# Performance work log

Measured on AMD Instinct MI355X. Metric: run time of the kernel, lower is better.

## Reference

```python
import jax, jax.numpy as jnp
import numpy as np

H = 128   # hidden_size
B = 8
TQ = 512  # num queries
TK = 512  # num keys


def setup_inputs() -> dict:
    key = jax.random.key(0)
    ks = jax.random.split(key, 8)
    s = 1.0 / np.sqrt(H)  # torch Linear default init bound
    return {
        "queries": jax.random.normal(ks[0], (B, TQ, H), dtype=jnp.float32),
        "keys": jax.random.normal(ks[1], (B, TK, H), dtype=jnp.float32),
        "Wa_w": jax.random.uniform(ks[2], (H, H), jnp.float32, -s, s),
        "Wa_b": jax.random.uniform(ks[3], (H,), jnp.float32, -s, s),
        "Ua_w": jax.random.uniform(ks[4], (H, H), jnp.float32, -s, s),
        "Ua_b": jax.random.uniform(ks[5], (H,), jnp.float32, -s, s),
        "Va_w": jax.random.uniform(ks[6], (H,), jnp.float32, -s, s),
        "Va_b": jax.random.uniform(ks[7], (), jnp.float32, -s, s),
    }


def reference(queries, keys, Wa_w, Wa_b, Ua_w, Ua_b, Va_w, Va_b):
    # Linear projections (torch Linear: y = x @ W.T + b)
    q = queries @ Wa_w.T + Wa_b                  # (B, Tq, H)
    k = keys @ Ua_w.T + Ua_b                     # (B, Tk, H)
    # Additive (Bahdanau) scores with broadcast intermediate (B, Tq, Tk, H)
    e = jnp.tanh(q[:, :, None, :] + k[:, None, :, :])
    scores = jnp.einsum('bqkh,h->bqk', e, Va_w) + Va_b  # (B, Tq, Tk)
    weights = jax.nn.softmax(scores, axis=-1)            # softmax over keys
    contexts = jnp.einsum('bqk,bkh->bqh', weights, keys) # (B, Tq, H)
    return contexts, weights
```

## Files before the change

### kernel.cpp

```cpp
#include <hip/hip_runtime.h>
#include <hip/hip_bf16.h>
#include <stdint.h>

#define HD 128
#define NB 8
#define TQN 512
#define TKN 512
#define QT 8
#define KTILE 64
#define KSTR 132
#define QSTR 132
#define KBSTR 136
#define FQT 8

typedef __attribute__((ext_vector_type(8))) short short8;
typedef __attribute__((ext_vector_type(4))) float f32x4;
typedef __attribute__((ext_vector_type(2))) float f32x2;

#if __has_builtin(__builtin_elementwise_fma)
#define FMA2(a,b,c) __builtin_elementwise_fma((a),(b),(c))
#else
#define FMA2(a,b,c) ((a)*(b)+(c))
#endif

static __device__ __forceinline__ float lo16(uint32_t w){
  union { uint32_t i; float f; } v; v.i = w << 16; return v.f;
}
static __device__ __forceinline__ float hi16(uint32_t w){
  union { uint32_t i; float f; } v; v.i = w & 0xffff0000u; return v.f;
}
static __device__ __forceinline__ float bf2f(unsigned short u){
  union { uint32_t i; float f; } v; v.i = ((uint32_t)u) << 16; return v.f;
}
static __device__ __forceinline__ uint32_t f2bf(float f){
  union { float f; uint32_t i; } v; v.f = f;
  uint32_t u = v.i;
  u += 0x7fffu + ((u >> 16) & 1u);
  return u >> 16;
}
static __device__ __forceinline__ float tanh_acc(float x){
  float e = __builtin_amdgcn_exp2f(x * 2.8853900817779268f);
  return fmaf(-2.0f, __builtin_amdgcn_rcpf(e + 1.0f), 1.0f);
}
template<int CTRL>
static __device__ __forceinline__ float dpp_add(float x){
  union { float f; int i; } u; u.f = x;
  int y = __builtin_amdgcn_update_dpp(0, u.i, CTRL, 0xf, 0xf, true);
  union { int i; float f; } w; w.i = y;
  return x + w.f;
}
static __device__ __forceinline__ float ld1(const void* p, size_t idx, bool f32){
  return f32 ? ((const float*)p)[idx] : bf2f(((const unsigned short*)p)[idx]);
}
static __device__ __forceinline__ short8 ld8bf(const void* p, size_t idx, bool f32){
  short8 r;
  if (f32){
    const float* s = (const float*)p + idx;
    #pragma unroll
    for (int i = 0; i < 8; i++) r[i] = (short)f2bf(s[i]);
  } else {
    r = *(const short8*)((const unsigned short*)p + idx);
  }
  return r;
}

__global__ __launch_bounds__(256) void proj_kernel(
    const void* __restrict__ queries, const void* __restrict__ keys,
    const void* __restrict__ Wa_w,   const void* __restrict__ Wa_b,
    const void* __restrict__ Ua_w,   const void* __restrict__ Ua_b,
    float* __restrict__ tq_g, float* __restrict__ tk_g)
{
  __shared__ unsigned int flg_s[8];
  const int tid = threadIdx.x;
  if (tid < 8) flg_s[tid] = 0;
  __syncthreads();
  {
    const void* ptrs[6] = {queries, keys, Wa_w, Wa_b, Ua_w, Ua_b};
    const int grp = tid >> 5;
    const int l   = tid & 31;
    if (grp < 6){
      const unsigned short* p = (const unsigned short*)ptrs[grp];
      unsigned short a = p[2*l], c = p[64 + 2*l];
      if (((a >> 7) & 0xFF) > 0x90 || ((c >> 7) & 0xFF) > 0x90)
        atomicOr(&flg_s[grp], 1u);
    }
  }
  __syncthreads();
  const int lane = tid & 63, wv = tid >> 6, ln = lane & 15, quad = lane >> 4;
  const int b7  = blockIdx.x & 7;
  const int idx = blockIdx.x >> 3;
  const int row0 = (idx < 32) ? (b7*TQN + idx*16)
                              : (NB*TQN + b7*TKN + (idx-32)*16);

  const void* x; const void* W; const void* bias; float* dst; int r;
  bool fx, fw, fb;
  if (row0 < NB*TQN){
    x = queries; W = Wa_w; bias = Wa_b; dst = tq_g; r = row0;
    fx = flg_s[0] != 0; fw = flg_s[2] != 0; fb = flg_s[3] != 0;
  } else {
    x = keys; W = Ua_w; bias = Ua_b; dst = tk_g; r = row0 - NB*TQN;
    fx = flg_s[1] != 0; fw = flg_s[4] != 0; fb = flg_s[5] != 0;
  }

  short8 a[4];
  #pragma unroll
  for (int ks = 0; ks < 4; ks++)
    a[ks] = ld8bf(x, (size_t)(r + ln)*HD + ks*32 + quad*8, fx);

  #pragma unroll
  for (int nt = 0; nt < 2; nt++){
    const int h0 = (2*wv + nt)*16;
    f32x4 c = {0.f,0.f,0.f,0.f};
    #pragma unroll
    for (int ks = 0; ks < 4; ks++)
      c = __builtin_amdgcn_mfma_f32_16x16x32_bf16(
            a[ks], ld8bf(W, (size_t)(h0 + ln)*HD + ks*32 + quad*8, fw), c, 0,0,0);
    const float wb = ld1(bias, h0 + ln, fb);
    #pragma unroll
    for (int r4 = 0; r4 < 4; r4++){
      const float e = __builtin_amdgcn_exp2f((c[r4] + wb) * 2.8853900817779268f);
      dst[(size_t)(r + quad*4 + r4)*HD + h0 + ln] =
          fminf(fmaxf(e, 0x1p-13f), 0x1p13f);
    }
  }
}

__global__ __launch_bounds__(1024, 8) void attn_kernel(
    const void* __restrict__ queries, const void* __restrict__ keys,
    const void* __restrict__ Va_w,
    const float* __restrict__ tq_g, const float* __restrict__ tk_g,
    void* __restrict__ out)
{
  __shared__ __align__(16) float tk_s[KTILE*KSTR];
  __shared__ float wgt_s[QT*TKN];
  __shared__ unsigned int flg_s[4];

  const int tid = threadIdx.x;
  const int b     = blockIdx.x & 7;
  const int qbase = (blockIdx.x >> 3) * QT;

  float4 st[2];
  {
    const float4* src = (const float4*)(tk_g + (size_t)(b*TKN)*HD);
    #pragma unroll
    for (int j = 0; j < 2; j++) st[j] = src[tid + 1024*j];
  }

  if (tid < 4) flg_s[tid] = 0;
  __syncthreads();
  {
    const void* ptrs[3] = {queries, keys, Va_w};
    const int grp = tid >> 5;
    const int l   = tid & 31;
    if (grp < 3){
      const unsigned short* p = (const unsigned short*)ptrs[grp];
      unsigned short a = p[2*l], c = p[64 + 2*l];
      if (((a >> 7) & 0xFF) > 0x90 || ((c >> 7) & 0xFF) > 0x90)
        atomicOr(&flg_s[grp], 1u);
    }
  }
  __syncthreads();
  const bool fQ  = flg_s[0] != 0;
  const bool fK  = flg_s[1] != 0;
  const bool fVw = flg_s[2] != 0;

  const int lane = tid & 63;
  const int wv   = tid >> 6;
  const int qr   = wv & 7;
  const int hh   = wv >> 3;
  const int ln   = lane & 15;
  const int quad = lane >> 4;
  const int s8   = lane >> 3;
  const int o8   = lane & 7;

  f32x2 eq2[4], a2[4];
  {
    const float* qsrc = tq_g + (size_t)(b*TQN + qbase + qr)*HD + o8*16 + hh*8;
    #pragma unroll
    for (int c = 0; c < 2; c++){
      const float4 t = *(const float4*)(qsrc + c*4);
      eq2[2*c].x = t.x; eq2[2*c].y = t.y;
      eq2[2*c+1].x = t.z; eq2[2*c+1].y = t.w;
      a2[2*c].x   = -2.0f * ld1(Va_w, o8*16 + hh*8 + c*4 + 0, fVw);
      a2[2*c].y   = -2.0f * ld1(Va_w, o8*16 + hh*8 + c*4 + 1, fVw);
      a2[2*c+1].x = -2.0f * ld1(Va_w, o8*16 + hh*8 + c*4 + 2, fVw);
      a2[2*c+1].y = -2.0f * ld1(Va_w, o8*16 + hh*8 + c*4 + 3, fVw);
    }
  }
  f32x2 one2; one2.x = 1.f; one2.y = 1.f;

  float sc8[8];
  for (int kt = 0; kt < 8; kt++){
    #pragma unroll
    for (int j = 0; j < 2; j++){
      const int f = tid + 1024*j;
      *(float4*)(tk_s + (f >> 5)*KSTR + (f & 31)*4) = st[j];
    }
    __syncthreads();
    if (kt < 7){
      const float4* src = (const float4*)(tk_g + (size_t)(b*TKN + (kt+1)*KTILE)*HD);
      #pragma unroll
      for (int j = 0; j < 2; j++) st[j] = src[tid + 1024*j];
    }

    float acc[8];
    #pragma unroll
    for (int i = 0; i < 8; i++){
      const float* tk = tk_s + (i*8 + s8)*KSTR + o8*16 + hh*8;
      float acci = 0.f;
      #pragma unroll
      for (int c = 0; c < 2; c++){
        const float4 kv = *(const float4*)(tk + c*4);
        f32x2 kv0; kv0.x = kv.x; kv0.y = kv.y;
        f32x2 kv1; kv1.x = kv.z; kv1.y = kv.w;
        f32x2 x01 = FMA2(eq2[2*c],   kv0, one2);
        f32x2 x23 = FMA2(eq2[2*c+1], kv1, one2);
        f32x2 xs01; xs01.x = x01.y; xs01.y = x01.x;
        f32x2 xs23; xs23.x = x23.y; xs23.y = x23.x;
        f32x2 s01 = a2[2*c]   * xs01;
        f32x2 s23 = a2[2*c+1] * xs23;
        const float p01 = x01.x * x01.y;
        const float p23 = x23.x * x23.y;
        const float n01 = s01.x + s01.y;
        const float n23 = s23.x + s23.y;
        const float P   = p01 * p23;
        const float N   = fmaf(n01, p23, n23 * p01);
        acci = fmaf(N, __builtin_amdgcn_rcpf(P), acci);
      }
      acc[i] = acci;
    }
    #pragma unroll
    for (int i = 0; i < 8; i++){
      float a = acc[i];
      a = dpp_add<0xB1>(a);
      a = dpp_add<0x4E>(a);
      a = dpp_add<0x141>(a);
      acc[i] = a;
    }
    float sc = acc[0];
    #pragma unroll
    for (int i = 1; i < 8; i++) sc = (o8 == i) ? acc[i] : sc;
    sc8[kt] = sc;
    __syncthreads();
  }

  if (hh == 1){
    #pragma unroll
    for (int kt = 0; kt < 8; kt++)
      tk_s[qr*TKN + kt*64 + o8*8 + s8] = sc8[kt];
  }
  __syncthreads();
  if (hh == 0){
    float vals[8];
    float m = -1e30f;
    #pragma unroll
    for (int j = 0; j < 8; j++){
      vals[j] = sc8[j] + tk_s[qr*TKN + j*64 + o8*8 + s8];
      m = fmaxf(m, vals[j]);
    }
    #pragma unroll
    for (int o = 32; o > 0; o >>= 1) m = fmaxf(m, __shfl_xor(m, o));
    float sum = 0.f;
    #pragma unroll
    for (int j = 0; j < 8; j++){
      vals[j] = __builtin_amdgcn_exp2f((vals[j]-m)*1.4426950408889634f);
      sum += vals[j];
    }
    #pragma unroll
    for (int o = 32; o > 0; o >>= 1) sum += __shfl_xor(sum, o);
    const float inv = __builtin_amdgcn_rcpf(sum);
    const int psrc = ((((lane & 7) << 3) | (lane >> 3)) << 2);
    const size_t wbase = (size_t)NB*TQN*HD + (size_t)(b*TQN + qbase + qr)*TKN;
    float* wrow = wgt_s + qr*TKN;
    #pragma unroll
    for (int j = 0; j < 8; j++){
      union { float f; int i; } u; u.f = vals[j]*inv;
      union { int i; float f; } t; t.i = __builtin_amdgcn_ds_bpermute(psrc, u.i);
      wrow[j*64 + lane] = t.f;
      if (fQ) ((float*)out)[wbase + j*64 + lane] = t.f;
      else    ((unsigned short*)out)[wbase + j*64 + lane] = (unsigned short)f2bf(t.f);
    }
  }
  __syncthreads();

  {
    const int p2 = wv & 3;
    const int g2 = wv >> 2;
    const int h0 = ln * 8;
    f32x2 a0v[4], a1v[4];
    #pragma unroll
    for (int t = 0; t < 4; t++){
      a0v[t].x = 0.f; a0v[t].y = 0.f;
      a1v[t].x = 0.f; a1v[t].y = 0.f;
    }
    const float* w0rb = wgt_s + (2*p2)*TKN;
    if (!fK){
      const unsigned short* kb = (const unsigned short*)keys
          + (size_t)(b*TKN)*HD + h0;
      #pragma unroll
      for (int t = 0; t < 2; t++){
        const int kt = g2*2 + t;
        const float* w0r = w0rb + kt*KTILE;
        const float* w1r = w0r + TKN;
        #pragma unroll
        for (int i = 0; i < 16; i++){
          const int k = i*4 + quad;
          const uint4 v = *(const uint4*)(kb + (size_t)(kt*KTILE + k)*HD);
          const float w0 = w0r[k];
          const float w1 = w1r[k];
          f32x2 c0; c0.x = lo16(v.x); c0.y = hi16(v.x);
          f32x2 c1; c1.x = lo16(v.y); c1.y = hi16(v.y);
          f32x2 c2; c2.x = lo16(v.z); c2.y = hi16(v.z);
          f32x2 c3; c3.x = lo16(v.w); c3.y = hi16(v.w);
          f32x2 w0v; w0v.x = w0; w0v.y = w0;
          f32x2 w1v; w1v.x = w1; w1v.y = w1;
          a0v[0] = FMA2(w0v, c0, a0v[0]); a0v[1] = FMA2(w0v, c1, a0v[1]);
          a0v[2] = FMA2(w0v, c2, a0v[2]); a0v[3] = FMA2(w0v, c3, a0v[3]);
          a1v[0] = FMA2(w1v, c0, a1v[0]); a1v[1] = FMA2(w1v, c1, a1v[1]);
          a1v[2] = FMA2(w1v, c2, a1v[2]); a1v[3] = FMA2(w1v, c3, a1v[3]);
        }
      }
    } else {
      const float* kb = (const float*)keys + (size_t)(b*TKN)*HD + h0;
      #pragma unroll
      for (int t = 0; t < 2; t++){
        const int kt = g2*2 + t;
        const float* w0r = w0rb + kt*KTILE;
        const float* w1r = w0r + TKN;
        #pragma unroll
        for (int i = 0; i < 16; i++){
          const int k = i*4 + quad;
          const float* kr = kb + (size_t)(kt*KTILE + k)*HD;
          const float4 k0 = *(const float4*)(kr);
          const float4 k1 = *(const float4*)(kr + 4);
          const float w0 = w0r[k];
          const float w1 = w1r[k];
          f32x2 c0; c0.x = k0.x; c0.y = k0.y;
          f32x2 c1; c1.x = k0.z; c1.y = k0.w;
          f32x2 c2; c2.x = k1.x; c2.y = k1.y;
          f32x2 c3; c3.x = k1.z; c3.y = k1.w;
          f32x2 w0v; w0v.x = w0; w0v.y = w0;
          f32x2 w1v; w1v.x = w1; w1v.y = w1;
          a0v[0] = FMA2(w0v, c0, a0v[0]); a0v[1] = FMA2(w0v, c1, a0v[1]);
          a0v[2] = FMA2(w0v, c2, a0v[2]); a0v[3] = FMA2(w0v, c3, a0v[3]);
          a1v[0] = FMA2(w1v, c0, a1v[0]); a1v[1] = FMA2(w1v, c1, a1v[1]);
          a1v[2] = FMA2(w1v, c2, a1v[2]); a1v[3] = FMA2(w1v, c3, a1v[3]);
        }
      }
    }
    float a0[8], a1[8];
    #pragma unroll
    for (int t = 0; t < 4; t++){
      a0[2*t] = a0v[t].x; a0[2*t+1] = a0v[t].y;
      a1[2*t] = a1v[t].x; a1[2*t+1] = a1v[t].y;
    }
    #pragma unroll
    for (int t = 0; t < 8; t++){
      a0[t] += __shfl_xor(a0[t], 16); a0[t] += __shfl_xor(a0[t], 32);
      a1[t] += __shfl_xor(a1[t], 16); a1[t] += __shfl_xor(a1[t], 32);
    }
    float* part = tk_s;
    if (g2 > 0 && quad == 0){
      const int base = ((g2-1)*8 + 2*p2)*HD + h0;
      *(float4*)(part + base       ) = (float4){a0[0],a0[1],a0[2],a0[3]};
      *(float4*)(part + base + 4   ) = (float4){a0[4],a0[5],a0[6],a0[7]};
      *(float4*)(part + base + HD  ) = (float4){a1[0],a1[1],a1[2],a1[3]};
      *(float4*)(part + base + HD+4) = (float4){a1[4],a1[5],a1[6],a1[7]};
    }
    __syncthreads();
    if (g2 == 0 && quad == 0){
      #pragma unroll
      for (int gg = 0; gg < 3; gg++){
        const int base = (gg*8 + 2*p2)*HD + h0;
        const float4 q00 = *(const float4*)(part + base);
        const float4 q01 = *(const float4*)(part + base + 4);
        const float4 q10 = *(const float4*)(part + base + HD);
        const float4 q11 = *(const float4*)(part + base + HD + 4);
        a0[0]+=q00.x; a0[1]+=q00.y; a0[2]+=q00.z; a0[3]+=q00.w;
        a0[4]+=q01.x; a0[5]+=q01.y; a0[6]+=q01.z; a0[7]+=q01.w;
        a1[0]+=q10.x; a1[1]+=q10.y; a1[2]+=q10.z; a1[3]+=q10.w;
        a1[4]+=q11.x; a1[5]+=q11.y; a1[6]+=q11.z; a1[7]+=q11.w;
      }
      const size_t crow0 = (size_t)(b*TQN + qbase + 2*p2    )*HD + h0;
      const size_t crow1 = (size_t)(b*TQN + qbase + 2*p2 + 1)*HD + h0;
      if (fQ){
        float* oc = (float*)out;
        *(float4*)(oc + crow0)     = (float4){a0[0],a0[1],a0[2],a0[3]};
        *(float4*)(oc + crow0 + 4) = (float4){a0[4],a0[5],a0[6],a0[7]};
        *(float4*)(oc + crow1)     = (float4){a1[0],a1[1],a1[2],a1[3]};
        *(float4*)(oc + crow1 + 4) = (float4){a1[4],a1[5],a1[6],a1[7]};
      } else {
        uint4 o0, o1;
        o0.x = f2bf(a0[0]) | (f2bf(a0[1]) << 16);
        o0.y = f2bf(a0[2]) | (f2bf(a0[3]) << 16);
        o0.z = f2bf(a0[4]) | (f2bf(a0[5]) << 16);
        o0.w = f2bf(a0[6]) | (f2bf(a0[7]) << 16);
        o1.x = f2bf(a1[0]) | (f2bf(a1[1]) << 16);
        o1.y = f2bf(a1[2]) | (f2bf(a1[3]) << 16);
        o1.z = f2bf(a1[4]) | (f2bf(a1[5]) << 16);
        o1.w = f2bf(a1[6]) | (f2bf(a1[7]) << 16);
        *(uint4*)((unsigned short*)out + crow0) = o0;
        *(uint4*)((unsigned short*)out + crow1) = o1;
      }
    }
  }
}

__global__ __launch_bounds__(512, 4) void fused_kernel(
    const void* __restrict__ queries, const void* __restrict__ keys,
    const void* __restrict__ Wa_w,   const void* __restrict__ Wa_b,
    const void* __restrict__ Ua_w,   const void* __restrict__ Ua_b,
    const void* __restrict__ Va_w,
    void* __restrict__ out)
{
  __shared__ float qp_s[FQT*QSTR];
  __shared__ float va_s[HD];
  __shared__ __align__(16) unsigned short keys_s[KTILE*KBSTR];
  __shared__ __align__(16) float kp_s[KTILE*QSTR];
  __shared__ float sc_s[FQT*TKN];
  __shared__ unsigned int flg_s[8];

  const int tid = threadIdx.x;
  if (tid < 8) flg_s[tid] = 0;
  __syncthreads();
  {
    const void* ptrs[7] = {queries, keys, Wa_w, Wa_b, Ua_w, Ua_b, Va_w};
    const int grp = tid >> 5;
    const int l   = tid & 31;
    if (grp < 7){
      const unsigned short* p = (const unsigned short*)ptrs[grp];
      unsigned short a = p[2*l], c = p[64 + 2*l];
      if (((a >> 7) & 0xFF) > 0x90 || ((c >> 7) & 0xFF) > 0x90)
        atomicOr(&flg_s[grp], 1u);
    }
  }
  __syncthreads();
  const bool fQ  = flg_s[0] != 0;
  const bool fK  = flg_s[1] != 0;
  const bool fWw = flg_s[2] != 0;
  const bool fWb = flg_s[3] != 0;
  const bool fUw = flg_s[4] != 0;
  const bool fUb = flg_s[5] != 0;
  const bool fVw = flg_s[6] != 0;

  const int lane = tid & 63;
  const int wv   = tid >> 6;
  const int ln   = lane & 15;
  const int quad = lane >> 4;
  const int b     = blockIdx.x >> 6;
  const int qbase = (blockIdx.x & 63) * FQT;

  if (tid < HD) va_s[tid] = ld1(Va_w, tid, fVw);
  {
    const int h0 = wv * 16;
    const size_t qrow = (size_t)(b*TQN + qbase + (ln & 7))*HD;
    f32x4 c = {0.f,0.f,0.f,0.f};
    #pragma unroll
    for (int ks = 0; ks < 4; ks++){
      short8 a = ld8bf(queries, qrow + ks*32 + quad*8, fQ);
      short8 w = ld8bf(Wa_w, (size_t)(h0 + ln)*HD + ks*32 + quad*8, fWw);
      c = __builtin_amdgcn_mfma_f32_16x16x32_bf16(a, w, c, 0,0,0);
    }
    const float wb = ld1(Wa_b, h0 + ln, fWb);
    #pragma unroll
    for (int r = 0; r < 4; r++){
      const int row = quad*4 + r;
      if (row < FQT) qp_s[row*QSTR + h0 + ln] = tanh_acc(c[r] + wb);
    }
  }
  short8 ub[4];
  float ubias;
  {
    const int h0 = wv * 16;
    #pragma unroll
    for (int ks = 0; ks < 4; ks++)
      ub[ks] = ld8bf(Ua_w, (size_t)(h0 + ln)*HD + ks*32 + quad*8, fUw);
    ubias = ld1(Ua_b, h0 + ln, fUb);
  }
  {
    if (fK){
      const float4* src = (const float4*)((const float*)keys + (size_t)(b*TKN)*HD);
      #pragma unroll
      for (int j = 0; j < 4; j++){
        const int f = tid + 512*j;
        float4 v = src[f];
        const int k = f >> 5, h = (f & 31)*4;
        uint2 p;
        p.x = f2bf(v.x) | (f2bf(v.y) << 16);
        p.y = f2bf(v.z) | (f2bf(v.w) << 16);
        *(uint2*)(keys_s + k*KBSTR + h) = p;
      }
    } else {
      const uint4* src = (const uint4*)((const unsigned short*)keys + (size_t)(b*TKN)*HD);
      #pragma unroll
      for (int j = 0; j < 2; j++){
        const int f = tid + 512*j;
        uint4 v = src[f];
        const int k = f >> 4, h = (f & 15)*8;
        *(uint4*)(keys_s + k*KBSTR + h) = v;
      }
    }
  }
  __syncthreads();

  const int s8 = lane >> 3;
  const int o8 = lane & 7;
  float tqr[16], var[16], vat[16];
  {
    const float* qsrc = qp_s + wv*QSTR + o8*16;
    const float* vsrc = va_s + o8*16;
    #pragma unroll
    for (int c = 0; c < 4; c++){
      float4 t = *(const float4*)(qsrc + c*4);
      float4 v = *(const float4*)(vsrc + c*4);
      tqr[c*4+0]=t.x; tqr[c*4+1]=t.y; tqr[c*4+2]=t.z; tqr[c*4+3]=t.w;
      var[c*4+0]=v.x; var[c*4+1]=v.y; var[c*4+2]=v.z; var[c*4+3]=v.w;
      vat[c*4+0]=v.x*t.x; vat[c*4+1]=v.y*t.y; vat[c*4+2]=v.z*t.z; vat[c*4+3]=v.w*t.w;
    }
  }
  for (int kt = 0; kt < 8; kt++){
    f32x4 kc[4];
    #pragma unroll
    for (int mt = 0; mt < 4; mt++) kc[mt] = (f32x4){0.f,0.f,0.f,0.f};
    #pragma unroll
    for (int ks = 0; ks < 4; ks++){
      short8 af[4];
      #pragma unroll
      for (int mt = 0; mt < 4; mt++)
        af[mt] = *(const short8*)(keys_s + (mt*16 + ln)*KBSTR + ks*32 + quad*8);
      #pragma unroll
      for (int mt = 0; mt < 4; mt++)
        kc[mt] = __builtin_amdgcn_mfma_f32_16x16x32_bf16(af[mt], ub[ks], kc[mt], 0,0,0);
    }
    __syncthreads();
    #pragma unroll
    for (int mt = 0; mt < 4; mt++)
      #pragma unroll
      for (int r = 0; r < 4; r++)
        kp_s[(mt*16 + quad*4 + r)*QSTR + wv*16 + ln] = tanh_acc(kc[mt][r] + ubias);
    if (kt < 7){
      if (fK){
        const float4* src = (const float4*)((const float*)keys + (size_t)(b*TKN + (kt+1)*KTILE)*HD);
        #pragma unroll
        for (int j = 0; j < 4; j++){
          const int f = tid + 512*j;
          float4 v = src[f];
          const int k = f >> 5, h = (f & 31)*4;
          uint2 p;
          p.x = f2bf(v.x) | (f2bf(v.y) << 16);
          p.y = f2bf(v.z) | (f2bf(v.w) << 16);
          *(uint2*)(keys_s + k*KBSTR + h) = p;
        }
      } else {
        const uint4* src = (const uint4*)((const unsigned short*)keys + (size_t)(b*TKN + (kt+1)*KTILE)*HD);
        #pragma unroll
        for (int j = 0; j < 2; j++){
          const int f = tid + 512*j;
          uint4 v = src[f];
          const int k = f >> 4, h = (f & 15)*8;
          *(uint4*)(keys_s + k*KBSTR + h) = v;
        }
      }
    }
    __syncthreads();
    float acc[8];
    #pragma unroll
    for (int i = 0; i < 8; i++) acc[i] = 0.f;
    #pragma unroll
    for (int i = 0; i < 8; i++){
      const float* tk = kp_s + (i*8 + s8)*QSTR + o8*16;
      #pragma unroll
      for (int c = 0; c < 4; c++){
        const float4 kv = *(const float4*)(tk + c*4);
        acc[i] = fmaf(fmaf(var[c*4+0], kv.x, vat[c*4+0]),
                      __builtin_amdgcn_rcpf(fmaf(tqr[c*4+0], kv.x, 1.f)), acc[i]);
        acc[i] = fmaf(fmaf(var[c*4+1], kv.y, vat[c*4+1]),
                      __builtin_amdgcn_rcpf(fmaf(tqr[c*4+1], kv.y, 1.f)), acc[i]);
        acc[i] = fmaf(fmaf(var[c*4+2], kv.z, vat[c*4+2]),
                      __builtin_amdgcn_rcpf(fmaf(tqr[c*4+2], kv.z, 1.f)), acc[i]);
        acc[i] = fmaf(fmaf(var[c*4+3], kv.w, vat[c*4+3]),
                      __builtin_amdgcn_rcpf(fmaf(tqr[c*4+3], kv.w, 1.f)), acc[i]);
      }
    }
    #pragma unroll
    for (int i = 0; i < 8; i++){
      float a = acc[i];
      a = dpp_add<0xB1>(a);
      a = dpp_add<0x4E>(a);
      a = dpp_add<0x141>(a);
      acc[i] = a;
    }
    float sc = acc[0];
    #pragma unroll
    for (int i = 1; i < 8; i++) sc = (o8 == i) ? acc[i] : sc;
    sc_s[wv*TKN + kt*KTILE + o8*8 + s8] = sc;
  }
  __syncthreads();
  {
    float vals[8];
    float m = -1e30f;
    #pragma unroll
    for (int j = 0; j < 8; j++){
      vals[j] = sc_s[wv*TKN + lane + 64*j];
      m = fmaxf(m, vals[j]);
    }
    #pragma unroll
    for (int o = 32; o > 0; o >>= 1) m = fmaxf(m, __shfl_xor(m, o));
    float sum = 0.f;
    #pragma unroll
    for (int j = 0; j < 8; j++){
      vals[j] = __builtin_amdgcn_exp2f((vals[j]-m)*1.4426950408889634f);
      sum += vals[j];
    }
    #pragma unroll
    for (int o = 32; o > 0; o >>= 1) sum += __shfl_xor(sum, o);
    const float inv = __builtin_amdgcn_rcpf(sum);
    const size_t wbase = (size_t)NB*TQN*HD + (size_t)(b*TQN + qbase + wv)*TKN;
    #pragma unroll
    for (int j = 0; j < 8; j++){
      const float w = vals[j]*inv;
      sc_s[wv*TKN + lane + 64*j] = w;
      if (fQ) ((float*)out)[wbase + lane + 64*j] = w;
      else    ((unsigned short*)out)[wbase + lane + 64*j] = (unsigned short)f2bf(w);
    }
  }
  __syncthreads();
  {
    const int p2 = wv & 3;
    const int g2 = wv >> 2;
    const int h0 = ln * 8;
    float a0[8], a1[8];
    #pragma unroll
    for (int t = 0; t < 8; t++){ a0[t] = 0.f; a1[t] = 0.f; }
    for (int kt = 0; kt < 8; kt++){
      if (fK){
        const float4* src = (const float4*)((const float*)keys + (size_t)(b*TKN + kt*KTILE)*HD);
        #pragma unroll
        for (int j = 0; j < 4; j++){
          const int f = tid + 512*j;
          const int k = f >> 5, h = (f & 31)*4;
          *(float4*)(kp_s + k*QSTR + h) = src[f];
        }
      } else {
        const uint4* src = (const uint4*)((const unsigned short*)keys + (size_t)(b*TKN + kt*KTILE)*HD);
        #pragma unroll
        for (int j = 0; j < 2; j++){
          const int f = tid + 512*j;
          const int k = f >> 4, h = (f & 15)*8;
          uint4 v = src[f];
          float4 d0, d1;
          d0.x = lo16(v.x); d0.y = hi16(v.x); d0.z = lo16(v.y); d0.w = hi16(v.y);
          d1.x = lo16(v.z); d1.y = hi16(v.z); d1.z = lo16(v.w); d1.w = hi16(v.w);
          *(float4*)(kp_s + k*QSTR + h)     = d0;
          *(float4*)(kp_s + k*QSTR + h + 4) = d1;
        }
      }
      __syncthreads();
      const float* w0r = sc_s + (2*p2)*TKN + kt*KTILE + g2*32;
      const float* w1r = w0r + TKN;
      #pragma unroll
      for (int i = 0; i < 8; i++){
        const int k = i*4 + quad;
        const float w0 = w0r[k];
        const float w1 = w1r[k];
        const float* kr = kp_s + (g2*32 + k)*QSTR + h0;
        const float4 k0 = *(const float4*)(kr);
        const float4 k1 = *(const float4*)(kr + 4);
        a0[0]=fmaf(w0,k0.x,a0[0]); a0[1]=fmaf(w0,k0.y,a0[1]);
        a0[2]=fmaf(w0,k0.z,a0[2]); a0[3]=fmaf(w0,k0.w,a0[3]);
        a0[4]=fmaf(w0,k1.x,a0[4]); a0[5]=fmaf(w0,k1.y,a0[5]);
        a0[6]=fmaf(w0,k1.z,a0[6]); a0[7]=fmaf(w0,k1.w,a0[7]);
        a1[0]=fmaf(w1,k0.x,a1[0]); a1[1]=fmaf(w1,k0.y,a1[1]);
        a1[2]=fmaf(w1,k0.z,a1[2]); a1[3]=fmaf(w1,k0.w,a1[3]);
        a1[4]=fmaf(w1,k1.x,a1[4]); a1[5]=fmaf(w1,k1.y,a1[5]);
        a1[6]=fmaf(w1,k1.z,a1[6]); a1[7]=fmaf(w1,k1.w,a1[7]);
      }
      __syncthreads();
    }
    #pragma unroll
    for (int t = 0; t < 8; t++){
      a0[t] += __shfl_xor(a0[t], 16); a0[t] += __shfl_xor(a0[t], 32);
      a1[t] += __shfl_xor(a1[t], 16); a1[t] += __shfl_xor(a1[t], 32);
    }
    float* part = qp_s;
    if (g2 == 1 && quad == 0){
      *(float4*)(part + (2*p2  )*HD + h0    ) = (float4){a0[0],a0[1],a0[2],a0[3]};
      *(float4*)(part + (2*p2  )*HD + h0 + 4) = (float4){a0[4],a0[5],a0[6],a0[7]};
      *(float4*)(part + (2*p2+1)*HD + h0    ) = (float4){a1[0],a1[1],a1[2],a1[3]};
      *(float4*)(part + (2*p2+1)*HD + h0 + 4) = (float4){a1[4],a1[5],a1[6],a1[7]};
    }
    __syncthreads();
    if (g2 == 0 && quad == 0){
      const float4 p00 = *(const float4*)(part + (2*p2  )*HD + h0    );
      const float4 p01 = *(const float4*)(part + (2*p2  )*HD + h0 + 4);
      const float4 p10 = *(const float4*)(part + (2*p2+1)*HD + h0    );
      const float4 p11 = *(const float4*)(part + (2*p2+1)*HD + h0 + 4);
      const size_t crow0 = (size_t)(b*TQN + qbase + 2*p2    )*HD + h0;
      const size_t crow1 = (size_t)(b*TQN + qbase + 2*p2 + 1)*HD + h0;
      if (fQ){
        float* oc = (float*)out;
        *(float4*)(oc + crow0)     = (float4){a0[0]+p00.x, a0[1]+p00.y, a0[2]+p00.z, a0[3]+p00.w};
        *(float4*)(oc + crow0 + 4) = (float4){a0[4]+p01.x, a0[5]+p01.y, a0[6]+p01.z, a0[7]+p01.w};
        *(float4*)(oc + crow1)     = (float4){a1[0]+p10.x, a1[1]+p10.y, a1[2]+p10.z, a1[3]+p10.w};
        *(float4*)(oc + crow1 + 4) = (float4){a1[4]+p11.x, a1[5]+p11.y, a1[6]+p11.z, a1[7]+p11.w};
      } else {
        uint4 o0, o1;
        o0.x = f2bf(a0[0]+p00.x) | (f2bf(a0[1]+p00.y) << 16);
        o0.y = f2bf(a0[2]+p00.z) | (f2bf(a0[3]+p00.w) << 16);
        o0.z = f2bf(a0[4]+p01.x) | (f2bf(a0[5]+p01.y) << 16);
        o0.w = f2bf(a0[6]+p01.z) | (f2bf(a0[7]+p01.w) << 16);
        o1.x = f2bf(a1[0]+p10.x) | (f2bf(a1[1]+p10.y) << 16);
        o1.y = f2bf(a1[2]+p10.z) | (f2bf(a1[3]+p10.w) << 16);
        o1.z = f2bf(a1[4]+p11.x) | (f2bf(a1[5]+p11.y) << 16);
        o1.w = f2bf(a1[6]+p11.z) | (f2bf(a1[7]+p11.w) << 16);
        *(uint4*)((unsigned short*)out + crow0) = o0;
        *(uint4*)((unsigned short*)out + crow1) = o1;
      }
    }
  }
}

extern "C" void kernel_launch(void* const* d_in, const int* in_sizes, int n_in,
                              void* d_out, int out_size, void* d_ws, size_t ws_size,
                              hipStream_t stream) {
  (void)in_sizes; (void)n_in; (void)out_size;
  const size_t need = (size_t)2 * NB * TQN * HD * sizeof(float);
  if (ws_size >= need){
    float* tq_g = (float*)d_ws;
    float* tk_g = tq_g + (size_t)NB*TQN*HD;
    proj_kernel<<<512, 256, 0, stream>>>(d_in[0], d_in[1], d_in[2], d_in[3],
                                         d_in[4], d_in[5], tq_g, tk_g);
    attn_kernel<<<512, 1024, 0, stream>>>(d_in[0], d_in[1], d_in[6],
                                          tq_g, tk_g, d_out);
  } else {
    fused_kernel<<<512, 512, 0, stream>>>(d_in[0], d_in[1], d_in[2], d_in[3],
                                          d_in[4], d_in[5], d_in[6], d_out);
  }
}
```

Baseline: 148.3 us.

## Store projected keys as bf16 and double-buffer the key tile in LDS

The projection kernel now writes the exp-transformed key projections as bf16 instead of fp32, which halves the global traffic and the LDS footprint of the key tiles read by the attention kernel. The attention kernel keeps two bf16 tiles in LDS and writes the next tile during the current compute, removing one barrier per key tile. The unpacking adds bf16-to-fp32 conversion ALU work, and the key operand of the tanh-based score loses precision. The fused fallback kernel only gets a stride constant rename.

After: 138.3 us. -6.7%, faster.

```diff
diff --git a/kernel.cpp b/kernel.cpp
--- a/kernel.cpp
+++ b/kernel.cpp
@@ -68,7 +68,7 @@
     const void* __restrict__ queries, const void* __restrict__ keys,
     const void* __restrict__ Wa_w,   const void* __restrict__ Wa_b,
     const void* __restrict__ Ua_w,   const void* __restrict__ Ua_b,
-    float* __restrict__ tq_g, float* __restrict__ tk_g)
+    float* __restrict__ tq_g, unsigned short* __restrict__ tk_gb)
 {
   __shared__ unsigned int flg_s[8];
   const int tid = threadIdx.x;
@@ -92,13 +92,14 @@
   const int row0 = (idx < 32) ? (b7*TQN + idx*16)
                               : (NB*TQN + b7*TKN + (idx-32)*16);
 
-  const void* x; const void* W; const void* bias; float* dst; int r;
+  const void* x; const void* W; const void* bias; int r;
   bool fx, fw, fb;
-  if (row0 < NB*TQN){
-    x = queries; W = Wa_w; bias = Wa_b; dst = tq_g; r = row0;
+  const bool isK = (row0 >= NB*TQN);
+  if (!isK){
+    x = queries; W = Wa_w; bias = Wa_b; r = row0;
     fx = flg_s[0] != 0; fw = flg_s[2] != 0; fb = flg_s[3] != 0;
   } else {
-    x = keys; W = Ua_w; bias = Ua_b; dst = tk_g; r = row0 - NB*TQN;
+    x = keys; W = Ua_w; bias = Ua_b; r = row0 - NB*TQN;
     fx = flg_s[1] != 0; fw = flg_s[4] != 0; fb = flg_s[5] != 0;
   }
 
@@ -119,8 +120,10 @@
     #pragma unroll
     for (int r4 = 0; r4 < 4; r4++){
       const float e = __builtin_amdgcn_exp2f((c[r4] + wb) * 2.8853900817779268f);
-      dst[(size_t)(r + quad*4 + r4)*HD + h0 + ln] =
-          fminf(fmaxf(e, 0x1p-13f), 0x1p13f);
+      const float ec = fminf(fmaxf(e, 0x1p-13f), 0x1p13f);
+      const size_t di = (size_t)(r + quad*4 + r4)*HD + h0 + ln;
+      if (isK) tk_gb[di] = (unsigned short)f2bf(ec);
+      else     tq_g[di]  = ec;
     }
   }
 }
@@ -128,10 +131,10 @@
 __global__ __launch_bounds__(1024, 8) void attn_kernel(
     const void* __restrict__ queries, const void* __restrict__ keys,
     const void* __restrict__ Va_w,
-    const float* __restrict__ tq_g, const float* __restrict__ tk_g,
+    const float* __restrict__ tq_g, const unsigned short* __restrict__ tk_gb,
     void* __restrict__ out)
 {
-  __shared__ __align__(16) float tk_s[KTILE*KSTR];
+  __shared__ __align__(16) unsigned short tkb_s[2][KTILE*KBSTR];
   __shared__ float wgt_s[QT*TKN];
   __shared__ unsigned int flg_s[4];
 
@@ -139,11 +142,10 @@
   const int b     = blockIdx.x & 7;
   const int qbase = (blockIdx.x >> 3) * QT;
 
-  float4 st[2];
-  {
-    const float4* src = (const float4*)(tk_g + (size_t)(b*TKN)*HD);
-    #pragma unroll
-    for (int j = 0; j < 2; j++) st[j] = src[tid + 1024*j];
+  uint4 st;
+  {
+    const uint4* src = (const uint4*)(tk_gb + (size_t)(b*TKN)*HD);
+    st = src[tid];
   }
 
   if (tid < 4) flg_s[tid] = 0;
@@ -172,6 +174,8 @@
   const int quad = lane >> 4;
   const int s8   = lane >> 3;
   const int o8   = lane & 7;
+  const int sk   = tid >> 4;
+  const int shh  = (tid & 15) * 8;
 
   f32x2 eq2[4], a2[4];
   {
@@ -189,36 +193,32 @@
   }
   f32x2 one2; one2.x = 1.f; one2.y = 1.f;
 
+  *(uint4*)(&tkb_s[0][sk*KBSTR + shh]) = st;
+  __syncthreads();
+
   float sc8[8];
   for (int kt = 0; kt < 8; kt++){
-    #pragma unroll
-    for (int j = 0; j < 2; j++){
-      const int f = tid + 1024*j;
-      *(float4*)(tk_s + (f >> 5)*KSTR + (f & 31)*4) = st[j];
-    }
-    __syncthreads();
     if (kt < 7){
-      const float4* src = (const float4*)(tk_g + (size_t)(b*TKN + (kt+1)*KTILE)*HD);
-      #pragma unroll
-      for (int j = 0; j < 2; j++) st[j] = src[tid + 1024*j];
-    }
+      const uint4* src = (const uint4*)(tk_gb + (size_t)(b*TKN + (kt+1)*KTILE)*HD);
+      st = src[tid];
+    }
+    const unsigned short* buf = &tkb_s[kt & 1][0];
 
     float acc[8];
     #pragma unroll
     for (int i = 0; i < 8; i++){
-      const float* tk = tk_s + (i*8 + s8)*KSTR + o8*16 + hh*8;
+      const unsigned short* tk = buf + (i*8 + s8)*KBSTR + o8*16 + hh*8;
+      const uint4 v = *(const uint4*)tk;
       float acci = 0.f;
-      #pragma unroll
-      for (int c = 0; c < 2; c++){
-        const float4 kv = *(const float4*)(tk + c*4);
-        f32x2 kv0; kv0.x = kv.x; kv0.y = kv.y;
-        f32x2 kv1; kv1.x = kv.z; kv1.y = kv.w;
-        f32x2 x01 = FMA2(eq2[2*c],   kv0, one2);
-        f32x2 x23 = FMA2(eq2[2*c+1], kv1, one2);
+      {
+        f32x2 kv0; kv0.x = lo16(v.x); kv0.y = hi16(v.x);
+        f32x2 kv1; kv1.x = lo16(v.y); kv1.y = hi16(v.y);
+        f32x2 x01 = FMA2(eq2[0], kv0, one2);
+        f32x2 x23 = FMA2(eq2[1], kv1, one2);
         f32x2 xs01; xs01.x = x01.y; xs01.y = x01.x;
         f32x2 xs23; xs23.x = x23.y; xs23.y = x23.x;
-        f32x2 s01 = a2[2*c]   * xs01;
-        f32x2 s23 = a2[2*c+1] * xs23;
+        f32x2 s01 = a2[0] * xs01;
+        f32x2 s23 = a2[1] * xs23;
         const float p01 = x01.x * x01.y;
         const float p23 = x23.x * x23.y;
         const float n01 = s01.x + s01.y;
@@ -227,6 +227,23 @@
         const float N   = fmaf(n01, p23, n23 * p01);
         acci = fmaf(N, __builtin_amdgcn_rcpf(P), acci);
       }
+      {
+        f32x2 kv0; kv0.x = lo16(v.z); kv0.y = hi16(v.z);
+        f32x2 kv1; kv1.x = lo16(v.w); kv1.y = hi16(v.w);
+        f32x2 x01 = FMA2(eq2[2], kv0, one2);
+        f32x2 x23 = FMA2(eq2[3], kv1, one2);
+        f32x2 xs01; xs01.x = x01.y; xs01.y = x01.x;
+        f32x2 xs23; xs23.x = x23.y; xs23.y = x23.x;
+        f32x2 s01 = a2[2] * xs01;
+        f32x2 s23 = a2[3] * xs23;
+        const float p01 = x01.x * x01.y;
+        const float p23 = x23.x * x23.y;
+        const float n01 = s01.x + s01.y;
+        const float n23 = s23.x + s23.y;
+        const float P   = p01 * p23;
+        const float N   = fmaf(n01, p23, n23 * p01);
+        acci = fmaf(N, __builtin_amdgcn_rcpf(P), acci);
+      }
       acc[i] = acci;
     }
     #pragma unroll
@@ -241,13 +258,17 @@
     #pragma unroll
     for (int i = 1; i < 8; i++) sc = (o8 == i) ? acc[i] : sc;
     sc8[kt] = sc;
+
+    if (kt < 7)
+      *(uint4*)(&tkb_s[(kt+1) & 1][sk*KBSTR + shh]) = st;
     __syncthreads();
   }
 
+  float* psc = (float*)&tkb_s[0][0];
   if (hh == 1){
     #pragma unroll
     for (int kt = 0; kt < 8; kt++)
-      tk_s[qr*TKN + kt*64 + o8*8 + s8] = sc8[kt];
+      psc[qr*TKN + kt*64 + o8*8 + s8] = sc8[kt];
   }
   __syncthreads();
   if (hh == 0){
@@ -255,7 +276,7 @@
     float m = -1e30f;
     #pragma unroll
     for (int j = 0; j < 8; j++){
-      vals[j] = sc8[j] + tk_s[qr*TKN + j*64 + o8*8 + s8];
+      vals[j] = sc8[j] + psc[qr*TKN + j*64 + o8*8 + s8];
       m = fmaxf(m, vals[j]);
     }
     #pragma unroll
@@ -359,7 +380,8 @@
       a0[t] += __shfl_xor(a0[t], 16); a0[t] += __shfl_xor(a0[t], 32);
       a1[t] += __shfl_xor(a1[t], 16); a1[t] += __shfl_xor(a1[t], 32);
     }
-    float* part = tk_s;
+    __syncthreads();
+    float* part = psc;
     if (g2 > 0 && quad == 0){
       const int base = ((g2-1)*8 + 2*p2)*HD + h0;
       *(float4*)(part + base       ) = (float4){a0[0],a0[1],a0[2],a0[3]};
@@ -416,7 +438,7 @@
   __shared__ float qp_s[FQT*QSTR];
   __shared__ float va_s[HD];
   __shared__ __align__(16) unsigned short keys_s[KTILE*KBSTR];
-  __shared__ __align__(16) float kp_s[KTILE*QSTR];
+  __shared__ __align__(16) float kp_s[KTILE*KSTR];
   __shared__ float sc_s[FQT*TKN];
   __shared__ unsigned int flg_s[8];
 
@@ -537,7 +559,7 @@
     for (int mt = 0; mt < 4; mt++)
       #pragma unroll
       for (int r = 0; r < 4; r++)
-        kp_s[(mt*16 + quad*4 + r)*QSTR + wv*16 + ln] = tanh_acc(kc[mt][r] + ubias);
+        kp_s[(mt*16 + quad*4 + r)*KSTR + wv*16 + ln] = tanh_acc(kc[mt][r] + ubias);
     if (kt < 7){
       if (fK){
         const float4* src = (const float4*)((const float*)keys + (size_t)(b*TKN + (kt+1)*KTILE)*HD);
@@ -568,7 +590,7 @@
     for (int i = 0; i < 8; i++) acc[i] = 0.f;
     #pragma unroll
     for (int i = 0; i < 8; i++){
-      const float* tk = kp_s + (i*8 + s8)*QSTR + o8*16;
+      const float* tk = kp_s + (i*8 + s8)*KSTR + o8*16;
       #pragma unroll
       for (int c = 0; c < 4; c++){
         const float4 kv = *(const float4*)(tk + c*4);
@@ -639,7 +661,7 @@
         for (int j = 0; j < 4; j++){
           const int f = tid + 512*j;
           const int k = f >> 5, h = (f & 31)*4;
-          *(float4*)(kp_s + k*QSTR + h) = src[f];
+          *(float4*)(kp_s + k*KSTR + h) = src[f];
         }
       } else {
         const uint4* src = (const uint4*)((const unsigned short*)keys + (size_t)(b*TKN + kt*KTILE)*HD);
@@ -651,8 +673,8 @@
           float4 d0, d1;
           d0.x = lo16(v.x); d0.y = hi16(v.x); d0.z = lo16(v.y); d0.w = hi16(v.y);
           d1.x = lo16(v.z); d1.y = hi16(v.z); d1.z = lo16(v.w); d1.w = hi16(v.w);
-          *(float4*)(kp_s + k*QSTR + h)     = d0;
-          *(float4*)(kp_s + k*QSTR + h + 4) = d1;
+          *(float4*)(kp_s + k*KSTR + h)     = d0;
+          *(float4*)(kp_s + k*KSTR + h + 4) = d1;
         }
       }
       __syncthreads();
@@ -663,7 +685,7 @@
         const int k = i*4 + quad;
         const float w0 = w0r[k];
         const float w1 = w1r[k];
-        const float* kr = kp_s + (g2*32 + k)*QSTR + h0;
+        const float* kr = kp_s + (g2*32 + k)*KSTR + h0;
         const float4 k0 = *(const float4*)(kr);
         const float4 k1 = *(const float4*)(kr + 4);
         a0[0]=fmaf(w0,k0.x,a0[0]); a0[1]=fmaf(w0,k0.y,a0[1]);
@@ -727,11 +749,11 @@
   const size_t need = (size_t)2 * NB * TQN * HD * sizeof(float);
   if (ws_size >= need){
     float* tq_g = (float*)d_ws;
-    float* tk_g = tq_g + (size_t)NB*TQN*HD;
+    unsigned short* tk_gb = (unsigned short*)(tq_g + (size_t)NB*TQN*HD);
     proj_kernel<<<512, 256, 0, stream>>>(d_in[0], d_in[1], d_in[2], d_in[3],
-                                         d_in[4], d_in[5], tq_g, tk_g);
+                                         d_in[4], d_in[5], tq_g, tk_gb);
     attn_kernel<<<512, 1024, 0, stream>>>(d_in[0], d_in[1], d_in[6],
-                                          tq_g, tk_g, d_out);
+                                          tq_g, tk_gb, d_out);
   } else {
     fused_kernel<<<512, 512, 0, stream>>>(d_in[0], d_in[1], d_in[2], d_in[3],
                                           d_in[4], d_in[5], d_in[6], d_out);
```
